# Kernel tuning notes

Hardware: AMD Instinct MI355X
Metric: run time of the kernel (lower is better)

## Reference

```python
import jax, jax.numpy as jnp
import numpy as np

H = 8
DK = 32
D_MODEL = H * DK


def _leaky(x):
    # LeakyReLU(negative_slope=0.1)
    return jnp.where(x > 0, x, 0.1 * x)


def _edge_feat(p_edge, W1, b1, W2, b2):
    # p_edge: [b, d_edge, n, n] -> [b, h, d_k, n, n]
    e = jnp.transpose(p_edge, (0, 2, 3, 1))          # [b, n, n, d_edge]
    e = _leaky(e @ W1 + b1) @ W2 + b2                # [b, n, n, d_model]
    b, n = e.shape[0], e.shape[1]
    e = e.reshape(b, n, n, H, DK)
    return jnp.transpose(e, (0, 3, 4, 1, 2))          # [b, h, d_k, n, n]


def setup_inputs() -> dict:
    key = jax.random.key(0)
    ks = jax.random.split(key, 24)
    b, n, d_model, d_edge, d_hidden = 2, 512, 256, 40, 32
    s = 0.05
    return {
        "query": jax.random.normal(ks[0], (b, n, d_model), jnp.float32),
        "key_": jax.random.normal(ks[1], (b, n, d_model), jnp.float32),
        "value": jax.random.normal(ks[2], (b, n, d_model), jnp.float32),
        "edges_att": jax.random.normal(ks[3], (b, d_edge, n, n), jnp.float32),
        "mask": jax.random.randint(ks[4], (b, n), 0, 2, jnp.int32),
        "Wq": jax.random.normal(ks[5], (d_model, d_model), jnp.float32) * s,
        "bq": jax.random.normal(ks[6], (d_model,), jnp.float32) * s,
        "Wk": jax.random.normal(ks[7], (d_model, d_model), jnp.float32) * s,
        "bk": jax.random.normal(ks[8], (d_model,), jnp.float32) * s,
        "Wv": jax.random.normal(ks[9], (d_model, d_model), jnp.float32) * s,
        "bv": jax.random.normal(ks[10], (d_model,), jnp.float32) * s,
        "Wo": jax.random.normal(ks[11], (d_model, d_model), jnp.float32) * s,
        "bo": jax.random.normal(ks[12], (d_model,), jnp.float32) * s,
        "rkW1": jax.random.normal(ks[13], (d_edge, d_hidden), jnp.float32) * s,
        "rkb1": jax.random.normal(ks[14], (d_hidden,), jnp.float32) * s,
        "rkW2": jax.random.normal(ks[15], (d_hidden, d_model), jnp.float32) * s,
        "rkb2": jax.random.normal(ks[16], (d_model,), jnp.float32) * s,
        "rvW1": jax.random.normal(ks[17], (d_edge, d_hidden), jnp.float32) * s,
        "rvb1": jax.random.normal(ks[18], (d_hidden,), jnp.float32) * s,
        "rvW2": jax.random.normal(ks[19], (d_hidden, d_model), jnp.float32) * s,
        "rvb2": jax.random.normal(ks[20], (d_model,), jnp.float32) * s,
        "u": jax.random.normal(ks[21], (H, DK), jnp.float32) * s,
        "v": jax.random.normal(ks[22], (H, DK), jnp.float32) * s,
    }


def reference(query, key_, value, edges_att, mask,
              Wq, bq, Wk, bk, Wv, bv, Wo, bo,
              rkW1, rkb1, rkW2, rkb2, rvW1, rvb1, rvW2, rvb2, u, v):
    b, n, _ = query.shape

    def proj(x, W, bb):
        return jnp.transpose((x @ W + bb).reshape(b, n, H, DK), (0, 2, 1, 3))  # [b,h,n,d_k]

    q = proj(query, Wq, bq)
    k = proj(key_, Wk, bk)
    val = proj(value, Wv, bv)

    relK = _edge_feat(edges_att, rkW1, rkb1, rkW2, rkb2)  # [b,h,d_k,n,n]
    relV = _edge_feat(edges_att, rvW1, rvb1, rvW2, rvb2)  # [b,h,d_k,n,n]

    inv = 1.0 / jnp.sqrt(jnp.asarray(DK, q.dtype))
    s1 = jnp.einsum('bhid,bhjd->bhij', q, k) * inv
    s2 = jnp.einsum('bhid,bhdij->bhij', q + k, relK) * inv
    s3 = jnp.einsum('bhid,hd->bhi', k, u)[..., None]      # broadcast over j
    s4 = jnp.einsum('bhdij,hd->bhij', relK, v)
    scores = s1 + s2 + s3 + s4
    scores = jnp.where(mask[:, None, None, :] == 0, jnp.asarray(-1e12, scores.dtype), scores)
    p = jax.nn.softmax(scores, axis=-1)                    # [b,h,n,n]

    o = jnp.einsum('bhij,bhjd->bhid', p, val) + jnp.einsum('bhij,bhdij->bhid', p, relV)
    x = jnp.transpose(o, (0, 2, 1, 3)).reshape(b, n, D_MODEL)
    return x @ Wo + bo
```

## Files before the change

kernel.cpp:

```cpp
#include <hip/hip_runtime.h>
#include <hip/hip_bf16.h>

#define HH 8
#define DKK 32
#define DM 256
#define NN 512
#define DE 40
#define DHID 32
#define CH 128

typedef __attribute__((ext_vector_type(4))) short short4v;
typedef __attribute__((ext_vector_type(8))) short short8v;
typedef __attribute__((ext_vector_type(4))) float f32x4;

__device__ __forceinline__ unsigned short f2bf(float x) {
    union { __hip_bfloat16 h; unsigned short u; } c;
    c.h = __float2bfloat16(x);
    return c.u;
}
__device__ __forceinline__ float bf2f(unsigned short u) {
    return __uint_as_float(((unsigned int)u) << 16);
}
__device__ __forceinline__ float bf_lo(unsigned int u){ return __uint_as_float(u << 16); }
__device__ __forceinline__ float bf_hi(unsigned int u){ return __uint_as_float(u & 0xffff0000u); }
__device__ __forceinline__ unsigned int pack2bf(float a, float b) {
    return (unsigned int)f2bf(a) | ((unsigned int)f2bf(b) << 16);
}
__device__ __forceinline__ short8v ld8(const unsigned short* p) {
    short4v lo = *(const short4v*)p;
    short4v hi = *(const short4v*)(p + 4);
    short8v r;
    r[0]=lo[0]; r[1]=lo[1]; r[2]=lo[2]; r[3]=lo[3];
    r[4]=hi[0]; r[5]=hi[1]; r[6]=hi[2]; r[7]=hi[3];
    return r;
}

__global__ __launch_bounds__(256) void w1_kernel(
    const float* __restrict__ rkW1, const float* __restrict__ rvW1,
    const float* __restrict__ rkb1, const float* __restrict__ rvb1,
    unsigned short* __restrict__ w1w, float* __restrict__ biasw)
{
    const int tid = threadIdx.x;
    const int n = tid >> 2, qd = tid & 3;
#pragma unroll
    for (int kk = 0; kk < 17; ++kk) {
        const int k = qd*17 + kk;
        float v = 0.f;
        if (k < DE) v = (n < 32) ? rkW1[k*DHID + n] : rvW1[k*DHID + (n-32)];
        w1w[n*68 + k] = f2bf(v);
    }
    if (tid < 64) biasw[tid] = (tid < 32) ? rkb1[tid] : rvb1[tid-32];
}

__global__ __launch_bounds__(256) void prep_kernel(
    const float* __restrict__ Q, const float* __restrict__ K,
    const float* __restrict__ vvec,
    const float* __restrict__ rkW2, const float* __restrict__ rkb2,
    float* __restrict__ gkw)
{
    const int bi = blockIdx.x;
    const int tid = threadIdx.x, h = tid >> 5, l32 = tid & 31;
    const float inv = 0.17677669529663687f;
    __shared__ __align__(16) float wf[DM];
    wf[tid] = inv*(Q[(size_t)bi*DM + tid] + K[(size_t)bi*DM + tid]) + vvec[tid];
    __syncthreads();
    float acc = 0.f;
#pragma unroll
    for (int d4 = 0; d4 < DKK/4; ++d4) {
        const float4 w4 = *(const float4*)(rkW2 + (size_t)l32*DM + h*DKK + d4*4);
        const float4 f4 = *(const float4*)(&wf[h*DKK + d4*4]);
        acc = fmaf(w4.x, f4.x, acc); acc = fmaf(w4.y, f4.y, acc);
        acc = fmaf(w4.z, f4.z, acc); acc = fmaf(w4.w, f4.w, acc);
    }
    gkw[(size_t)bi*264 + tid] = acc;
    if (tid < HH) {
        float a2 = 0.f;
#pragma unroll
        for (int d = 0; d < DKK; ++d)
            a2 = fmaf(rkb2[tid*DKK + d], wf[tid*DKK + d], a2);
        gkw[(size_t)bi*264 + 256 + tid] = a2;
    }
}

__global__ __launch_bounds__(256) void proj_kernel(
    const float* __restrict__ query, const float* __restrict__ key_,
    const float* __restrict__ value,
    const float* __restrict__ Wq, const float* __restrict__ bq,
    const float* __restrict__ Wk, const float* __restrict__ bk,
    const float* __restrict__ Wv, const float* __restrict__ bv,
    float* __restrict__ Q, float* __restrict__ K, float* __restrict__ V,
    int grpPerMat)
{
    const int m  = blockIdx.x / grpPerMat;
    const int r0 = (blockIdx.x % grpPerMat) * 4;
    const float* x; const float* W; const float* bb; float* dst;
    if (m == 0)      { x = query; W = Wq; bb = bq; dst = Q; }
    else if (m == 1) { x = key_;  W = Wk; bb = bk; dst = K; }
    else             { x = value; W = Wv; bb = bv; dst = V; }
    const int c = threadIdx.x;
    const float b0 = bb[c];
    float a0 = b0, a1 = b0, a2 = b0, a3 = b0;
    for (int k = 0; k < DM; ++k) {
        const float w = W[k*DM + c];
        a0 = fmaf(x[(size_t)(r0+0)*DM + k], w, a0);
        a1 = fmaf(x[(size_t)(r0+1)*DM + k], w, a1);
        a2 = fmaf(x[(size_t)(r0+2)*DM + k], w, a2);
        a3 = fmaf(x[(size_t)(r0+3)*DM + k], w, a3);
    }
    dst[(size_t)(r0+0)*DM + c] = a0;
    dst[(size_t)(r0+1)*DM + c] = a1;
    dst[(size_t)(r0+2)*DM + c] = a2;
    dst[(size_t)(r0+3)*DM + c] = a3;
}

__global__ __launch_bounds__(256) void s1_kernel(
    const float* __restrict__ Q, const float* __restrict__ K,
    unsigned short* __restrict__ s1)
{
    const int tid = threadIdx.x;
    const int bh = blockIdx.y, b = bh >> 3, hh = bh & 7;
    const int ti = (blockIdx.x >> 3) * 64, tj = (blockIdx.x & 7) * 64;
    __shared__ float Qt[64][33];
    __shared__ float Kt[64][33];
    const int c = tid & 31, r0 = tid >> 5;
#pragma unroll
    for (int s = 0; s < 8; ++s) {
        Qt[r0 + 8*s][c] = Q[(size_t)(b*NN + ti + r0 + 8*s)*DM + hh*DKK + c];
        Kt[r0 + 8*s][c] = K[(size_t)(b*NN + tj + r0 + 8*s)*DM + hh*DKK + c];
    }
    __syncthreads();
    const int tx = tid & 15, ty = tid >> 4;
    float acc[4][4] = {};
#pragma unroll
    for (int k = 0; k < DKK; ++k) {
        float qv[4], kv[4];
#pragma unroll
        for (int u = 0; u < 4; ++u) { qv[u] = Qt[ty*4+u][k]; kv[u] = Kt[tx*4+u][k]; }
#pragma unroll
        for (int ri = 0; ri < 4; ++ri)
#pragma unroll
            for (int cj = 0; cj < 4; ++cj)
                acc[ri][cj] = fmaf(qv[ri], kv[cj], acc[ri][cj]);
    }
    const float inv = 0.17677669529663687f;
#pragma unroll
    for (int ri = 0; ri < 4; ++ri) {
        ushort4 o;
        o.x = f2bf(acc[ri][0]*inv); o.y = f2bf(acc[ri][1]*inv);
        o.z = f2bf(acc[ri][2]*inv); o.w = f2bf(acc[ri][3]*inv);
        *(ushort4*)(s1 + ((size_t)(b*HH + hh)*NN + ti + ty*4 + ri)*NN + tj + tx*4) = o;
    }
}

__global__ __launch_bounds__(256, 5) void chunk_kernel(
    const float* __restrict__ edges, const int* __restrict__ mask,
    const float* __restrict__ vvec,
    const float* __restrict__ Q, const float* __restrict__ K, const float* __restrict__ V,
    const unsigned short* __restrict__ s1u,
    const unsigned short* __restrict__ w1w, const float* __restrict__ biasw,
    const float* __restrict__ gkw,
    float* __restrict__ ws_m, float* __restrict__ ws_z,
    float* __restrict__ ws_A, float* __restrict__ ws_O)
{
    const int bid = blockIdx.x;
    const int bi = bid >> 2, cq = bid & 3;
    const int b  = bi >> 9;
    const int i  = bi & 511;
    const int j0 = cq*CH;
    const int tid = threadIdx.x;
    const int h = tid >> 5, l32 = tid & 31;
    const int wid = tid >> 6, lane = tid & 63;
    const int g = lane >> 4, q16 = lane & 15;
    const int team = tid >> 6, qq = tid & 63, hq = qq >> 3;
    const int jj = tid & 127, half = tid >> 7;

    __shared__ __align__(16) unsigned char uni[17408];
    __shared__ __align__(16) unsigned short W1bf[64*68];
    __shared__ __align__(16) float sc[HH*132];
    __shared__ __align__(16) float gKs[HH*DKK];
    __shared__ float c0Ks[HH];
    __shared__ float bias_l[64];

    unsigned short* E   = (unsigned short*)uni;
    unsigned short* hvT = (unsigned short*)uni;
    unsigned short* hk  = (unsigned short*)(uni + 8448);
    unsigned short* pb  = (unsigned short*)(uni + 8448);
    float* paccA = (float*)uni;
    float* po    = (float*)(uni + 4096);

    const size_t ebase = (size_t)b*DE*NN*NN + (size_t)i*NN;

    float ev[20];
    {
        const float* ep = edges + ebase + j0 + jj;
#pragma unroll
        for (int u = 0; u < 20; ++u) ev[u] = ep[(size_t)(half*20+u)*NN*NN];
    }

    {
        const unsigned int* src = (const unsigned int*)w1w;
        unsigned int* dst = (unsigned int*)W1bf;
#pragma unroll
        for (int u = tid; u < 2176; u += 256) dst[u] = src[u];
        const float* gsrc = gkw + (size_t)bi*264;
        gKs[tid] = gsrc[tid];
        if (tid < HH) c0Ks[tid] = gsrc[256 + tid];
        if (tid < 64) bias_l[tid] = biasw[tid];
    }
    __syncthreads();

    float biasv[4];
#pragma unroll
    for (int nt = 0; nt < 4; ++nt) biasv[nt] = bias_l[nt*16 + q16];

    const float* vb = V + (size_t)b*NN*DM;
    const unsigned short* s1b = s1u + (size_t)b*HH*NN*NN + (size_t)i*NN;

    {
        unsigned int* Ed = (unsigned int*)&E[jj*68 + half*20];
#pragma unroll
        for (int u = 0; u < 10; ++u) Ed[u] = pack2bf(ev[2*u], ev[2*u+1]);
        if (half) {
            unsigned int* Ez = (unsigned int*)&E[jj*68 + 40];
#pragma unroll
            for (int z = 0; z < 12; ++z) Ez[z] = 0u;
        }
    }
    __syncthreads();

    f32x4 acc[2][4];
#pragma unroll
    for (int jt = 0; jt < 2; ++jt) {
        const int jn = wid*32 + jt*16 + q16;
        short8v a0 = ld8(&E[jn*68 + g*8]);
        short8v a1 = ld8(&E[jn*68 + 32 + g*8]);
#pragma unroll
        for (int nt = 0; nt < 4; ++nt) {
            const unsigned short* wp = &W1bf[(q16 + nt*16)*68 + g*8];
            f32x4 c;
            c[0] = biasv[nt]; c[1] = biasv[nt]; c[2] = biasv[nt]; c[3] = biasv[nt];
            c = __builtin_amdgcn_mfma_f32_16x16x32_bf16(a0, ld8(wp), c, 0, 0, 0);
            c = __builtin_amdgcn_mfma_f32_16x16x32_bf16(a1, ld8(wp + 32), c, 0, 0, 0);
            acc[jt][nt] = c;
        }
    }
    __syncthreads();

#pragma unroll
    for (int jt = 0; jt < 2; ++jt) {
        const int jw = wid*32 + jt*16 + g*4;
#pragma unroll
        for (int nt = 0; nt < 4; ++nt) {
#pragma unroll
            for (int r = 0; r < 4; ++r) {
                float x = acc[jt][nt][r];
                x = x > 0.f ? x : 0.1f*x;
                const unsigned short us = f2bf(x);
                const int n = nt*16 + q16;
                if (n < 32) hk[(jw+r)*34 + n] = us;
                else        hvT[(n-32)*132 + (jw+r)] = us;
            }
        }
    }
    __syncthreads();

    {
        unsigned int hku[16];
#pragma unroll
        for (int d = 0; d < 16; ++d) hku[d] = *(const unsigned int*)&hk[jj*34 + 2*d];
        const int mk = mask[b*NN + j0 + jj];
        float racc[4];
#pragma unroll
        for (int u = 0; u < 4; ++u) racc[u] = c0Ks[half*4 + u];
#pragma unroll
        for (int d = 0; d < 16; ++d) {
            const float lo = bf_lo(hku[d]), hi = bf_hi(hku[d]);
#pragma unroll
            for (int u = 0; u < 4; ++u) {
                const int hh = half*4 + u;
                racc[u] = fmaf(gKs[hh*DKK + 2*d],     lo, racc[u]);
                racc[u] = fmaf(gKs[hh*DKK + 2*d + 1], hi, racc[u]);
            }
        }
#pragma unroll
        for (int u = 0; u < 4; ++u) {
            const int hh = half*4 + u;
            float r = racc[u] + bf2f(s1b[(size_t)hh*NN*NN + j0 + jj]);
            if (mk == 0) r = -1e12f;
            sc[hh*132 + jj] = r;
        }
    }
    __syncthreads();

    {
        float sv[4];
        float mc = -3e38f;
#pragma unroll
        for (int k = 0; k < 4; ++k) { sv[k] = sc[h*132 + l32 + 32*k]; mc = fmaxf(mc, sv[k]); }
#pragma unroll
        for (int off = 16; off; off >>= 1) mc = fmaxf(mc, __shfl_xor(mc, off, 32));
        float zc = 0.f;
#pragma unroll
        for (int k = 0; k < 4; ++k) {
            const float e = __expf(sv[k] - mc);
            pb[h*132 + l32 + 32*k] = f2bf(e);
            zc += e;
        }
#pragma unroll
        for (int off = 16; off; off >>= 1) zc += __shfl_xor(zc, off, 32);
        if (l32 == 0) {
            ws_m[(size_t)bid*8 + h] = mc;
            ws_z[(size_t)bid*8 + h] = zc;
        }
    }
    __syncthreads();

    f32x4 accAf0 = {0.f,0.f,0.f,0.f}, accAf1 = {0.f,0.f,0.f,0.f};
    float aO0 = 0.f, aO1 = 0.f, aO2 = 0.f, aO3 = 0.f;
    {
        short8v pA = ld8(&pb[q16*132 + wid*32 + g*8]);
        short8v b0 = ld8(&hvT[q16*132 + wid*32 + g*8]);
        short8v b1 = ld8(&hvT[(16+q16)*132 + wid*32 + g*8]);
        accAf0 = __builtin_amdgcn_mfma_f32_16x16x32_bf16(pA, b0, accAf0, 0, 0, 0);
        accAf1 = __builtin_amdgcn_mfma_f32_16x16x32_bf16(pA, b1, accAf1, 0, 0, 0);

        const float* vrow = vb + (size_t)(j0 + team)*DM + qq*4;
        const unsigned short* ph = pb + hq*132 + team;
#pragma unroll 4
        for (int it = 0; it < 32; ++it) {
            const float p = bf2f(ph[4*it]);
            const float4 v4 = *(const float4*)(vrow + (size_t)it*4*DM);
            aO0 = fmaf(p, v4.x, aO0); aO1 = fmaf(p, v4.y, aO1);
            aO2 = fmaf(p, v4.z, aO2); aO3 = fmaf(p, v4.w, aO3);
        }
    }
    __syncthreads();

    if (g < 2) {
#pragma unroll
        for (int r = 0; r < 4; ++r) {
            paccA[wid*256 + (4*g+r)*32 + q16]      = accAf0[r];
            paccA[wid*256 + (4*g+r)*32 + 16 + q16] = accAf1[r];
        }
    }
    *(float4*)(po + team*256 + qq*4) = make_float4(aO0, aO1, aO2, aO3);
    __syncthreads();

    ws_A[(size_t)bid*256 + tid] = paccA[tid] + paccA[256+tid] + paccA[512+tid] + paccA[768+tid];
    ws_O[(size_t)bid*256 + tid] = po[tid] + po[256+tid] + po[512+tid] + po[768+tid];
}

__global__ __launch_bounds__(256) void combine_kernel(
    const float* __restrict__ rvW2, const float* __restrict__ rvb2,
    const float* __restrict__ Wo, const float* __restrict__ bo,
    const float* __restrict__ ws_m, const float* __restrict__ ws_z,
    const float* __restrict__ ws_A, const float* __restrict__ ws_O,
    float* __restrict__ out)
{
    const int bi0 = blockIdx.x * 2;
    const int tid = threadIdx.x;
    const int h = tid >> 5;
    __shared__ float A_l[2][DM], o_l[2][DM];
    __shared__ float wqs[2][4][HH], rzs[2][HH];

    if (tid < 16) {
        const int r = tid >> 3, hh = tid & 7;
        const int bi = bi0 + r;
        float mv[4], zv[4];
#pragma unroll
        for (int q = 0; q < 4; ++q) {
            mv[q] = ws_m[(size_t)(bi*4+q)*8 + hh];
            zv[q] = ws_z[(size_t)(bi*4+q)*8 + hh];
        }
        const float mm = fmaxf(fmaxf(mv[0], mv[1]), fmaxf(mv[2], mv[3]));
        float zt = 0.f;
#pragma unroll
        for (int q = 0; q < 4; ++q) {
            const float w = __expf(mv[q] - mm);
            wqs[r][q][hh] = w;
            zt = fmaf(zv[q], w, zt);
        }
        rzs[r][hh] = 1.f / zt;
    }
    __syncthreads();

    float o1v[2];
#pragma unroll
    for (int r = 0; r < 2; ++r) {
        const int bi = bi0 + r;
        const float rz = rzs[r][h];
        float A = 0.f, o1 = 0.f;
#pragma unroll
        for (int q = 0; q < 4; ++q) {
            const float w = wqs[r][q][h];
            A  = fmaf(w, ws_A[(size_t)(bi*4+q)*256 + tid], A);
            o1 = fmaf(w, ws_O[(size_t)(bi*4+q)*256 + tid], o1);
        }
        A_l[r][tid] = A * rz;
        o1v[r] = o1 * rz;
    }
    __syncthreads();

#pragma unroll
    for (int r = 0; r < 2; ++r) {
        float o2 = rvb2[tid];
#pragma unroll
        for (int t = 0; t < DHID; ++t)
            o2 = fmaf(A_l[r][h*DKK + t], rvW2[(size_t)t*DM + tid], o2);
        o_l[r][tid] = o1v[r] + o2;
    }
    __syncthreads();

    float acc0 = bo[tid], acc1 = acc0;
#pragma unroll 4
    for (int k = 0; k < DM; ++k) {
        const float w = Wo[(size_t)k*DM + tid];
        acc0 = fmaf(o_l[0][k], w, acc0);
        acc1 = fmaf(o_l[1][k], w, acc1);
    }
    out[(size_t)(bi0+0)*DM + tid] = acc0;
    out[(size_t)(bi0+1)*DM + tid] = acc1;
}

extern "C" void kernel_launch(void* const* d_in, const int* in_sizes, int n_in,
                              void* d_out, int out_size, void* d_ws, size_t ws_size,
                              hipStream_t stream) {
    const float* query = (const float*)d_in[0];
    const float* key_  = (const float*)d_in[1];
    const float* value = (const float*)d_in[2];
    const float* edges = (const float*)d_in[3];
    const int*   mask  = (const int*)d_in[4];
    const float* Wq = (const float*)d_in[5];
    const float* bq = (const float*)d_in[6];
    const float* Wk = (const float*)d_in[7];
    const float* bk = (const float*)d_in[8];
    const float* Wv = (const float*)d_in[9];
    const float* bv = (const float*)d_in[10];
    const float* Wo = (const float*)d_in[11];
    const float* bo = (const float*)d_in[12];
    const float* rkW1 = (const float*)d_in[13];
    const float* rkb1 = (const float*)d_in[14];
    const float* rkW2 = (const float*)d_in[15];
    const float* rkb2 = (const float*)d_in[16];
    const float* rvW1 = (const float*)d_in[17];
    const float* rvb1 = (const float*)d_in[18];
    const float* rvW2 = (const float*)d_in[19];
    const float* rvb2 = (const float*)d_in[20];
    const float* vvec = (const float*)d_in[22];

    const int rows = in_sizes[0] / DM;
    const int nchunk = rows * 4;

    float* Qw = (float*)d_ws;
    float* Kw = Qw + (size_t)rows*DM;
    float* Vw = Kw + (size_t)rows*DM;
    unsigned short* s1u = (unsigned short*)(Vw + (size_t)rows*DM);
    float* ws_m = (float*)(s1u + (size_t)2*HH*NN*NN);
    float* ws_z = ws_m + (size_t)nchunk*8;
    float* ws_A = ws_z + (size_t)nchunk*8;
    float* ws_O = ws_A + (size_t)nchunk*256;
    unsigned short* w1w = (unsigned short*)(ws_O + (size_t)nchunk*256);
    float* biasw = (float*)(w1w + 64*68 + 32);
    float* gkw   = biasw + 64;

    hipLaunchKernelGGL(w1_kernel, dim3(1), dim3(256), 0, stream,
                       rkW1, rvW1, rkb1, rvb1, w1w, biasw);
    hipLaunchKernelGGL(proj_kernel, dim3(3*rows/4), dim3(256), 0, stream,
                       query, key_, value, Wq, bq, Wk, bk, Wv, bv, Qw, Kw, Vw, rows/4);
    hipLaunchKernelGGL(s1_kernel, dim3(64, 16), dim3(256), 0, stream,
                       Qw, Kw, s1u);
    hipLaunchKernelGGL(prep_kernel, dim3(rows), dim3(256), 0, stream,
                       Qw, Kw, vvec, rkW2, rkb2, gkw);
    hipLaunchKernelGGL(chunk_kernel, dim3(nchunk), dim3(256), 0, stream,
                       edges, mask, vvec, Qw, Kw, Vw, s1u, w1w, biasw, gkw,
                       ws_m, ws_z, ws_A, ws_O);
    hipLaunchKernelGGL(combine_kernel, dim3(rows/2), dim3(256), 0, stream,
                       rvW2, rvb2, Wo, bo, ws_m, ws_z, ws_A, ws_O, (float*)d_out);
}
```

Measured before the change: 107.6 us.

## Split chunk kernel into edge-MLP stage and full-row attention with MFMA PV

Replaces the split-softmax chunk kernel plus combine kernel with two stages. The edge-MLP kernel writes full scores and the transposed hidden relV activations to workspace. A per-row attention kernel then does the exact softmax over all 512 keys and uses bf16 MFMA for P·V against a new transposed bf16 V written by the projection kernel. It also drops the W1 staging into LDS, reading weights directly from global. This trades the partial max/sum merge for extra global traffic of scores and hidden activations, and lowers V precision to bf16.

```diff
diff --git a/kernel.cpp b/kernel.cpp
--- a/kernel.cpp
+++ b/kernel.cpp
@@ -89,7 +89,7 @@
     const float* __restrict__ Wk, const float* __restrict__ bk,
     const float* __restrict__ Wv, const float* __restrict__ bv,
     float* __restrict__ Q, float* __restrict__ K, float* __restrict__ V,
-    int grpPerMat)
+    unsigned short* __restrict__ VbfT, int grpPerMat)
 {
     const int m  = blockIdx.x / grpPerMat;
     const int r0 = (blockIdx.x % grpPerMat) * 4;
@@ -111,6 +111,12 @@
     dst[(size_t)(r0+1)*DM + c] = a1;
     dst[(size_t)(r0+2)*DM + c] = a2;
     dst[(size_t)(r0+3)*DM + c] = a3;
+    if (m == 2) {
+        const int b = r0 >> 9, n0 = r0 & 511;
+        unsigned int* vt = (unsigned int*)(VbfT + ((size_t)(b*DM + c))*NN + n0);
+        vt[0] = pack2bf(a0, a1);
+        vt[1] = pack2bf(a2, a3);
+    }
 }
 
 __global__ __launch_bounds__(256) void s1_kernel(
@@ -152,41 +158,28 @@
     }
 }
 
-__global__ __launch_bounds__(256, 5) void chunk_kernel(
+__global__ __launch_bounds__(256, 5) void mlp_kernel(
     const float* __restrict__ edges, const int* __restrict__ mask,
-    const float* __restrict__ vvec,
-    const float* __restrict__ Q, const float* __restrict__ K, const float* __restrict__ V,
-    const unsigned short* __restrict__ s1u,
     const unsigned short* __restrict__ w1w, const float* __restrict__ biasw,
-    const float* __restrict__ gkw,
-    float* __restrict__ ws_m, float* __restrict__ ws_z,
-    float* __restrict__ ws_A, float* __restrict__ ws_O)
+    const float* __restrict__ gkw, const unsigned short* __restrict__ s1u,
+    float* __restrict__ s12, unsigned short* __restrict__ h1vT)
 {
     const int bid = blockIdx.x;
     const int bi = bid >> 2, cq = bid & 3;
-    const int b  = bi >> 9;
-    const int i  = bi & 511;
+    const int b  = bi >> 9, i = bi & 511;
     const int j0 = cq*CH;
     const int tid = threadIdx.x;
-    const int h = tid >> 5, l32 = tid & 31;
     const int wid = tid >> 6, lane = tid & 63;
     const int g = lane >> 4, q16 = lane & 15;
-    const int team = tid >> 6, qq = tid & 63, hq = qq >> 3;
     const int jj = tid & 127, half = tid >> 7;
 
     __shared__ __align__(16) unsigned char uni[17408];
-    __shared__ __align__(16) unsigned short W1bf[64*68];
-    __shared__ __align__(16) float sc[HH*132];
     __shared__ __align__(16) float gKs[HH*DKK];
     __shared__ float c0Ks[HH];
-    __shared__ float bias_l[64];
 
     unsigned short* E   = (unsigned short*)uni;
     unsigned short* hvT = (unsigned short*)uni;
     unsigned short* hk  = (unsigned short*)(uni + 8448);
-    unsigned short* pb  = (unsigned short*)(uni + 8448);
-    float* paccA = (float*)uni;
-    float* po    = (float*)(uni + 4096);
 
     const size_t ebase = (size_t)b*DE*NN*NN + (size_t)i*NN;
 
@@ -196,25 +189,14 @@
 #pragma unroll
         for (int u = 0; u < 20; ++u) ev[u] = ep[(size_t)(half*20+u)*NN*NN];
     }
-
-    {
-        const unsigned int* src = (const unsigned int*)w1w;
-        unsigned int* dst = (unsigned int*)W1bf;
-#pragma unroll
-        for (int u = tid; u < 2176; u += 256) dst[u] = src[u];
+    {
         const float* gsrc = gkw + (size_t)bi*264;
         gKs[tid] = gsrc[tid];
         if (tid < HH) c0Ks[tid] = gsrc[256 + tid];
-        if (tid < 64) bias_l[tid] = biasw[tid];
-    }
-    __syncthreads();
-
+    }
     float biasv[4];
 #pragma unroll
-    for (int nt = 0; nt < 4; ++nt) biasv[nt] = bias_l[nt*16 + q16];
-
-    const float* vb = V + (size_t)b*NN*DM;
-    const unsigned short* s1b = s1u + (size_t)b*HH*NN*NN + (size_t)i*NN;
+    for (int nt = 0; nt < 4; ++nt) biasv[nt] = biasw[nt*16 + q16];
 
     {
         unsigned int* Ed = (unsigned int*)&E[jj*68 + half*20];
@@ -236,7 +218,7 @@
         short8v a1 = ld8(&E[jn*68 + 32 + g*8]);
 #pragma unroll
         for (int nt = 0; nt < 4; ++nt) {
-            const unsigned short* wp = &W1bf[(q16 + nt*16)*68 + g*8];
+            const unsigned short* wp = w1w + (q16 + nt*16)*68 + g*8;
             f32x4 c;
             c[0] = biasv[nt]; c[1] = biasv[nt]; c[2] = biasv[nt]; c[3] = biasv[nt];
             c = __builtin_amdgcn_mfma_f32_16x16x32_bf16(a0, ld8(wp), c, 0, 0, 0);
@@ -269,6 +251,7 @@
 #pragma unroll
         for (int d = 0; d < 16; ++d) hku[d] = *(const unsigned int*)&hk[jj*34 + 2*d];
         const int mk = mask[b*NN + j0 + jj];
+        const unsigned short* s1b = s1u + (size_t)b*HH*NN*NN + (size_t)i*NN;
         float racc[4];
 #pragma unroll
         for (int u = 0; u < 4; ++u) racc[u] = c0Ks[half*4 + u];
@@ -287,139 +270,125 @@
             const int hh = half*4 + u;
             float r = racc[u] + bf2f(s1b[(size_t)hh*NN*NN + j0 + jj]);
             if (mk == 0) r = -1e12f;
-            sc[hh*132 + jj] = r;
-        }
-    }
-    __syncthreads();
-
-    {
-        float sv[4];
+            s12[(size_t)bi*4096 + hh*512 + j0 + jj] = r;
+        }
+    }
+    {
+        const int t = tid >> 3, c8 = tid & 7;
+        const unsigned int* src = (const unsigned int*)(hvT + t*132);
+        unsigned int* dst = (unsigned int*)(h1vT + ((size_t)bi*DHID + t)*NN + j0);
+#pragma unroll
+        for (int u = 0; u < 8; ++u) dst[c8*8 + u] = src[c8*8 + u];
+    }
+}
+
+__global__ __launch_bounds__(256, 4) void attn2_kernel(
+    const float* __restrict__ s12, const unsigned short* __restrict__ h1vT,
+    const unsigned short* __restrict__ VbfT,
+    const float* __restrict__ rvW2, const float* __restrict__ rvb2,
+    const float* __restrict__ Wo, const float* __restrict__ bo,
+    float* __restrict__ out)
+{
+    const int bi = blockIdx.x;
+    const int b  = bi >> 9;
+    const int tid = threadIdx.x;
+    const int h = tid >> 5, l32 = tid & 31;
+    const int wid = tid >> 6, lane = tid & 63;
+    const int g = lane >> 4, q16 = lane & 15;
+
+    __shared__ __align__(16) unsigned short pb[8*520];
+    __shared__ __align__(16) float paccA[4*256];
+    __shared__ __align__(16) float A_l[DM];
+    __shared__ __align__(16) float o_l[DM];
+    __shared__ float rz_s[HH];
+
+    {
+        float sv[16];
+        const float* srow = s12 + (size_t)bi*4096 + h*512 + l32;
+#pragma unroll
+        for (int k = 0; k < 16; ++k) sv[k] = srow[32*k];
         float mc = -3e38f;
 #pragma unroll
-        for (int k = 0; k < 4; ++k) { sv[k] = sc[h*132 + l32 + 32*k]; mc = fmaxf(mc, sv[k]); }
+        for (int k = 0; k < 16; ++k) mc = fmaxf(mc, sv[k]);
 #pragma unroll
         for (int off = 16; off; off >>= 1) mc = fmaxf(mc, __shfl_xor(mc, off, 32));
         float zc = 0.f;
 #pragma unroll
-        for (int k = 0; k < 4; ++k) {
+        for (int k = 0; k < 16; ++k) {
             const float e = __expf(sv[k] - mc);
-            pb[h*132 + l32 + 32*k] = f2bf(e);
+            pb[h*520 + l32 + 32*k] = f2bf(e);
             zc += e;
         }
 #pragma unroll
         for (int off = 16; off; off >>= 1) zc += __shfl_xor(zc, off, 32);
-        if (l32 == 0) {
-            ws_m[(size_t)bid*8 + h] = mc;
-            ws_z[(size_t)bid*8 + h] = zc;
-        }
-    }
-    __syncthreads();
-
-    f32x4 accAf0 = {0.f,0.f,0.f,0.f}, accAf1 = {0.f,0.f,0.f,0.f};
-    float aO0 = 0.f, aO1 = 0.f, aO2 = 0.f, aO3 = 0.f;
-    {
-        short8v pA = ld8(&pb[q16*132 + wid*32 + g*8]);
-        short8v b0 = ld8(&hvT[q16*132 + wid*32 + g*8]);
-        short8v b1 = ld8(&hvT[(16+q16)*132 + wid*32 + g*8]);
-        accAf0 = __builtin_amdgcn_mfma_f32_16x16x32_bf16(pA, b0, accAf0, 0, 0, 0);
-        accAf1 = __builtin_amdgcn_mfma_f32_16x16x32_bf16(pA, b1, accAf1, 0, 0, 0);
-
-        const float* vrow = vb + (size_t)(j0 + team)*DM + qq*4;
-        const unsigned short* ph = pb + hq*132 + team;
+        if (l32 == 0) rz_s[h] = 1.f / zc;
+    }
+    __syncthreads();
+
+    f32x4 co[4] = {{0,0,0,0},{0,0,0,0},{0,0,0,0},{0,0,0,0}};
+    f32x4 ca[2] = {{0,0,0,0},{0,0,0,0}};
+    {
+        const unsigned short* vbase = VbfT + (size_t)b*DM*NN;
 #pragma unroll 4
-        for (int it = 0; it < 32; ++it) {
-            const float p = bf2f(ph[4*it]);
-            const float4 v4 = *(const float4*)(vrow + (size_t)it*4*DM);
-            aO0 = fmaf(p, v4.x, aO0); aO1 = fmaf(p, v4.y, aO1);
-            aO2 = fmaf(p, v4.z, aO2); aO3 = fmaf(p, v4.w, aO3);
-        }
-    }
-    __syncthreads();
-
-    if (g < 2) {
-#pragma unroll
-        for (int r = 0; r < 4; ++r) {
-            paccA[wid*256 + (4*g+r)*32 + q16]      = accAf0[r];
-            paccA[wid*256 + (4*g+r)*32 + 16 + q16] = accAf1[r];
-        }
-    }
-    *(float4*)(po + team*256 + qq*4) = make_float4(aO0, aO1, aO2, aO3);
-    __syncthreads();
-
-    ws_A[(size_t)bid*256 + tid] = paccA[tid] + paccA[256+tid] + paccA[512+tid] + paccA[768+tid];
-    ws_O[(size_t)bid*256 + tid] = po[tid] + po[256+tid] + po[512+tid] + po[768+tid];
-}
-
-__global__ __launch_bounds__(256) void combine_kernel(
-    const float* __restrict__ rvW2, const float* __restrict__ rvb2,
-    const float* __restrict__ Wo, const float* __restrict__ bo,
-    const float* __restrict__ ws_m, const float* __restrict__ ws_z,
-    const float* __restrict__ ws_A, const float* __restrict__ ws_O,
-    float* __restrict__ out)
-{
-    const int bi0 = blockIdx.x * 2;
-    const int tid = threadIdx.x;
-    const int h = tid >> 5;
-    __shared__ float A_l[2][DM], o_l[2][DM];
-    __shared__ float wqs[2][4][HH], rzs[2][HH];
-
-    if (tid < 16) {
-        const int r = tid >> 3, hh = tid & 7;
-        const int bi = bi0 + r;
-        float mv[4], zv[4];
-#pragma unroll
-        for (int q = 0; q < 4; ++q) {
-            mv[q] = ws_m[(size_t)(bi*4+q)*8 + hh];
-            zv[q] = ws_z[(size_t)(bi*4+q)*8 + hh];
-        }
-        const float mm = fmaxf(fmaxf(mv[0], mv[1]), fmaxf(mv[2], mv[3]));
-        float zt = 0.f;
-#pragma unroll
-        for (int q = 0; q < 4; ++q) {
-            const float w = __expf(mv[q] - mm);
-            wqs[r][q][hh] = w;
-            zt = fmaf(zv[q], w, zt);
-        }
-        rzs[r][hh] = 1.f / zt;
-    }
-    __syncthreads();
-
-    float o1v[2];
-#pragma unroll
-    for (int r = 0; r < 2; ++r) {
-        const int bi = bi0 + r;
-        const float rz = rzs[r][h];
-        float A = 0.f, o1 = 0.f;
-#pragma unroll
-        for (int q = 0; q < 4; ++q) {
-            const float w = wqs[r][q][h];
-            A  = fmaf(w, ws_A[(size_t)(bi*4+q)*256 + tid], A);
-            o1 = fmaf(w, ws_O[(size_t)(bi*4+q)*256 + tid], o1);
-        }
-        A_l[r][tid] = A * rz;
-        o1v[r] = o1 * rz;
-    }
-    __syncthreads();
-
-#pragma unroll
-    for (int r = 0; r < 2; ++r) {
+        for (int ks = 0; ks < 16; ++ks) {
+            short8v pA = ld8(&pb[(lane & 7)*520 + ks*32 + g*8]);
+#pragma unroll
+            for (int nt = 0; nt < 4; ++nt) {
+                const int c = wid*64 + nt*16 + q16;
+                short8v bv = ld8(&vbase[(size_t)c*NN + ks*32 + g*8]);
+                co[nt] = __builtin_amdgcn_mfma_f32_16x16x32_bf16(pA, bv, co[nt], 0, 0, 0);
+            }
+        }
+        const unsigned short* habase = h1vT + (size_t)bi*DHID*NN;
+#pragma unroll
+        for (int kq = 0; kq < 4; ++kq) {
+            const int ks = wid*4 + kq;
+            short8v pA = ld8(&pb[(lane & 7)*520 + ks*32 + g*8]);
+#pragma unroll
+            for (int nt2 = 0; nt2 < 2; ++nt2) {
+                short8v hb = ld8(&habase[(size_t)(nt2*16 + q16)*NN + ks*32 + g*8]);
+                ca[nt2] = __builtin_amdgcn_mfma_f32_16x16x32_bf16(pA, hb, ca[nt2], 0, 0, 0);
+            }
+        }
+        if (g < 2) {
+#pragma unroll
+            for (int r = 0; r < 4; ++r) {
+                const int hrow = g*4 + r;
+                paccA[wid*256 + hrow*32 + q16]      = ca[0][r];
+                paccA[wid*256 + hrow*32 + 16 + q16] = ca[1][r];
+            }
+        }
+    }
+    __syncthreads();
+
+    A_l[tid] = (paccA[tid] + paccA[256+tid] + paccA[512+tid] + paccA[768+tid]) * rz_s[tid>>5];
+#pragma unroll
+    for (int nt = 0; nt < 4; ++nt) {
+        const int hc = wid*2 + (nt >> 1);
+        if (g == (hc >> 2)) {
+            const int c = wid*64 + nt*16 + q16;
+            o_l[c] = co[nt][hc & 3] * rz_s[hc];
+        }
+    }
+    __syncthreads();
+
+    {
         float o2 = rvb2[tid];
+        const int hb2 = tid >> 5;
 #pragma unroll
         for (int t = 0; t < DHID; ++t)
-            o2 = fmaf(A_l[r][h*DKK + t], rvW2[(size_t)t*DM + tid], o2);
-        o_l[r][tid] = o1v[r] + o2;
-    }
-    __syncthreads();
-
-    float acc0 = bo[tid], acc1 = acc0;
+            o2 = fmaf(A_l[hb2*DKK + t], rvW2[(size_t)t*DM + tid], o2);
+        o_l[tid] += o2;
+    }
+    __syncthreads();
+
+    {
+        float accw = bo[tid];
 #pragma unroll 4
-    for (int k = 0; k < DM; ++k) {
-        const float w = Wo[(size_t)k*DM + tid];
-        acc0 = fmaf(o_l[0][k], w, acc0);
-        acc1 = fmaf(o_l[1][k], w, acc1);
-    }
-    out[(size_t)(bi0+0)*DM + tid] = acc0;
-    out[(size_t)(bi0+1)*DM + tid] = acc1;
+        for (int k = 0; k < DM; ++k)
+            accw = fmaf(o_l[k], Wo[(size_t)k*DM + tid], accw);
+        out[(size_t)bi*DM + tid] = accw;
+    }
 }
 
 extern "C" void kernel_launch(void* const* d_in, const int* in_sizes, int n_in,
@@ -449,31 +418,29 @@
     const float* vvec = (const float*)d_in[22];
 
     const int rows = in_sizes[0] / DM;
-    const int nchunk = rows * 4;
-
-    float* Qw = (float*)d_ws;
-    float* Kw = Qw + (size_t)rows*DM;
-    float* Vw = Kw + (size_t)rows*DM;
-    unsigned short* s1u = (unsigned short*)(Vw + (size_t)rows*DM);
-    float* ws_m = (float*)(s1u + (size_t)2*HH*NN*NN);
-    float* ws_z = ws_m + (size_t)nchunk*8;
-    float* ws_A = ws_z + (size_t)nchunk*8;
-    float* ws_O = ws_A + (size_t)nchunk*256;
-    unsigned short* w1w = (unsigned short*)(ws_O + (size_t)nchunk*256);
-    float* biasw = (float*)(w1w + 64*68 + 32);
+
+    float* Qw   = (float*)d_ws;
+    float* Kw   = Qw  + (size_t)rows*DM;
+    float* Vw   = Kw  + (size_t)rows*DM;
+    float* s12w = Vw  + (size_t)rows*DM;
+    float* biasw = s12w + (size_t)rows*4096;
     float* gkw   = biasw + 64;
+    unsigned short* s1u  = (unsigned short*)(gkw + (size_t)rows*264);
+    unsigned short* VbfT = s1u + (size_t)2*HH*NN*NN;
+    unsigned short* w1w  = VbfT + (size_t)2*DM*NN;
+    unsigned short* h1vT = w1w + 64*68;
 
     hipLaunchKernelGGL(w1_kernel, dim3(1), dim3(256), 0, stream,
                        rkW1, rvW1, rkb1, rvb1, w1w, biasw);
     hipLaunchKernelGGL(proj_kernel, dim3(3*rows/4), dim3(256), 0, stream,
-                       query, key_, value, Wq, bq, Wk, bk, Wv, bv, Qw, Kw, Vw, rows/4);
+                       query, key_, value, Wq, bq, Wk, bk, Wv, bv,
+                       Qw, Kw, Vw, VbfT, rows/4);
     hipLaunchKernelGGL(s1_kernel, dim3(64, 16), dim3(256), 0, stream,
                        Qw, Kw, s1u);
     hipLaunchKernelGGL(prep_kernel, dim3(rows), dim3(256), 0, stream,
                        Qw, Kw, vvec, rkW2, rkb2, gkw);
-    hipLaunchKernelGGL(chunk_kernel, dim3(nchunk), dim3(256), 0, stream,
-                       edges, mask, vvec, Qw, Kw, Vw, s1u, w1w, biasw, gkw,
-                       ws_m, ws_z, ws_A, ws_O);
-    hipLaunchKernelGGL(combine_kernel, dim3(rows/2), dim3(256), 0, stream,
-                       rvW2, rvb2, Wo, bo, ws_m, ws_z, ws_A, ws_O, (float*)d_out);
-}
+    hipLaunchKernelGGL(mlp_kernel, dim3(rows*4), dim3(256), 0, stream,
+                       edges, mask, w1w, biasw, gkw, s1u, s12w, h1vT);
+    hipLaunchKernelGGL(attn2_kernel, dim3(rows), dim3(256), 0, stream,
+                       s12w, h1vT, VbfT, rvW2, rvb2, Wo, bo, (float*)d_out);
+}
```

Result: slower. 125.5 us (+16.6%).

## Use MFMA for P·V with transposed bf16 V and merge prep kernels

Applied to the files above, without the earlier changes.

The projection kernel now also writes V as a transposed bf16 array. The chunk kernel computes the per-head P·V product with bf16 MFMA over that array, replacing the scalar fp32 FMA loop and its shared-memory reduction; only the diagonal head blocks are stored. The s1, prep and w1 kernels are merged into one launch that picks its role by block index, saving two launches. The MFMA path computes all heads against all value columns and discards off-diagonal blocks, and bf16 V lowers precision.

```diff
diff --git a/kernel.cpp b/kernel.cpp
--- a/kernel.cpp
+++ b/kernel.cpp
@@ -35,53 +35,6 @@
     return r;
 }
 
-__global__ __launch_bounds__(256) void w1_kernel(
-    const float* __restrict__ rkW1, const float* __restrict__ rvW1,
-    const float* __restrict__ rkb1, const float* __restrict__ rvb1,
-    unsigned short* __restrict__ w1w, float* __restrict__ biasw)
-{
-    const int tid = threadIdx.x;
-    const int n = tid >> 2, qd = tid & 3;
-#pragma unroll
-    for (int kk = 0; kk < 17; ++kk) {
-        const int k = qd*17 + kk;
-        float v = 0.f;
-        if (k < DE) v = (n < 32) ? rkW1[k*DHID + n] : rvW1[k*DHID + (n-32)];
-        w1w[n*68 + k] = f2bf(v);
-    }
-    if (tid < 64) biasw[tid] = (tid < 32) ? rkb1[tid] : rvb1[tid-32];
-}
-
-__global__ __launch_bounds__(256) void prep_kernel(
-    const float* __restrict__ Q, const float* __restrict__ K,
-    const float* __restrict__ vvec,
-    const float* __restrict__ rkW2, const float* __restrict__ rkb2,
-    float* __restrict__ gkw)
-{
-    const int bi = blockIdx.x;
-    const int tid = threadIdx.x, h = tid >> 5, l32 = tid & 31;
-    const float inv = 0.17677669529663687f;
-    __shared__ __align__(16) float wf[DM];
-    wf[tid] = inv*(Q[(size_t)bi*DM + tid] + K[(size_t)bi*DM + tid]) + vvec[tid];
-    __syncthreads();
-    float acc = 0.f;
-#pragma unroll
-    for (int d4 = 0; d4 < DKK/4; ++d4) {
-        const float4 w4 = *(const float4*)(rkW2 + (size_t)l32*DM + h*DKK + d4*4);
-        const float4 f4 = *(const float4*)(&wf[h*DKK + d4*4]);
-        acc = fmaf(w4.x, f4.x, acc); acc = fmaf(w4.y, f4.y, acc);
-        acc = fmaf(w4.z, f4.z, acc); acc = fmaf(w4.w, f4.w, acc);
-    }
-    gkw[(size_t)bi*264 + tid] = acc;
-    if (tid < HH) {
-        float a2 = 0.f;
-#pragma unroll
-        for (int d = 0; d < DKK; ++d)
-            a2 = fmaf(rkb2[tid*DKK + d], wf[tid*DKK + d], a2);
-        gkw[(size_t)bi*264 + 256 + tid] = a2;
-    }
-}
-
 __global__ __launch_bounds__(256) void proj_kernel(
     const float* __restrict__ query, const float* __restrict__ key_,
     const float* __restrict__ value,
@@ -89,7 +42,7 @@
     const float* __restrict__ Wk, const float* __restrict__ bk,
     const float* __restrict__ Wv, const float* __restrict__ bv,
     float* __restrict__ Q, float* __restrict__ K, float* __restrict__ V,
-    int grpPerMat)
+    unsigned short* __restrict__ VbfT, int grpPerMat)
 {
     const int m  = blockIdx.x / grpPerMat;
     const int r0 = (blockIdx.x % grpPerMat) * 4;
@@ -111,51 +64,100 @@
     dst[(size_t)(r0+1)*DM + c] = a1;
     dst[(size_t)(r0+2)*DM + c] = a2;
     dst[(size_t)(r0+3)*DM + c] = a3;
-}
-
-__global__ __launch_bounds__(256) void s1_kernel(
+    if (m == 2) {
+        const int b = r0 >> 9, n0 = r0 & 511;
+        unsigned int* vt = (unsigned int*)(VbfT + ((size_t)(b*DM + c))*NN + n0);
+        vt[0] = pack2bf(a0, a1);
+        vt[1] = pack2bf(a2, a3);
+    }
+}
+
+__global__ __launch_bounds__(256) void pre_kernel(
     const float* __restrict__ Q, const float* __restrict__ K,
-    unsigned short* __restrict__ s1)
+    const float* __restrict__ vvec,
+    const float* __restrict__ rkW2, const float* __restrict__ rkb2,
+    const float* __restrict__ rkW1, const float* __restrict__ rvW1,
+    const float* __restrict__ rkb1, const float* __restrict__ rvb1,
+    unsigned short* __restrict__ s1, float* __restrict__ gkw,
+    unsigned short* __restrict__ w1w, float* __restrict__ biasw)
 {
+    const int bid = blockIdx.x;
     const int tid = threadIdx.x;
-    const int bh = blockIdx.y, b = bh >> 3, hh = bh & 7;
-    const int ti = (blockIdx.x >> 3) * 64, tj = (blockIdx.x & 7) * 64;
-    __shared__ float Qt[64][33];
-    __shared__ float Kt[64][33];
-    const int c = tid & 31, r0 = tid >> 5;
-#pragma unroll
-    for (int s = 0; s < 8; ++s) {
-        Qt[r0 + 8*s][c] = Q[(size_t)(b*NN + ti + r0 + 8*s)*DM + hh*DKK + c];
-        Kt[r0 + 8*s][c] = K[(size_t)(b*NN + tj + r0 + 8*s)*DM + hh*DKK + c];
-    }
-    __syncthreads();
-    const int tx = tid & 15, ty = tid >> 4;
-    float acc[4][4] = {};
-#pragma unroll
-    for (int k = 0; k < DKK; ++k) {
-        float qv[4], kv[4];
-#pragma unroll
-        for (int u = 0; u < 4; ++u) { qv[u] = Qt[ty*4+u][k]; kv[u] = Kt[tx*4+u][k]; }
-#pragma unroll
-        for (int ri = 0; ri < 4; ++ri)
-#pragma unroll
-            for (int cj = 0; cj < 4; ++cj)
-                acc[ri][cj] = fmaf(qv[ri], kv[cj], acc[ri][cj]);
-    }
-    const float inv = 0.17677669529663687f;
-#pragma unroll
-    for (int ri = 0; ri < 4; ++ri) {
-        ushort4 o;
-        o.x = f2bf(acc[ri][0]*inv); o.y = f2bf(acc[ri][1]*inv);
-        o.z = f2bf(acc[ri][2]*inv); o.w = f2bf(acc[ri][3]*inv);
-        *(ushort4*)(s1 + ((size_t)(b*HH + hh)*NN + ti + ty*4 + ri)*NN + tj + tx*4) = o;
+    __shared__ __align__(16) float sh[2*64*33];
+
+    if (bid < 1024) {
+        float (*Qt)[33] = (float(*)[33])sh;
+        float (*Kt)[33] = (float(*)[33])(sh + 64*33);
+        const int bh = bid >> 6, b = bh >> 3, hh = bh & 7;
+        const int bx = bid & 63;
+        const int ti = (bx >> 3) * 64, tj = (bx & 7) * 64;
+        const int c = tid & 31, r0 = tid >> 5;
+#pragma unroll
+        for (int s = 0; s < 8; ++s) {
+            Qt[r0 + 8*s][c] = Q[(size_t)(b*NN + ti + r0 + 8*s)*DM + hh*DKK + c];
+            Kt[r0 + 8*s][c] = K[(size_t)(b*NN + tj + r0 + 8*s)*DM + hh*DKK + c];
+        }
+        __syncthreads();
+        const int tx = tid & 15, ty = tid >> 4;
+        float acc[4][4] = {};
+#pragma unroll
+        for (int k = 0; k < DKK; ++k) {
+            float qv[4], kv[4];
+#pragma unroll
+            for (int u = 0; u < 4; ++u) { qv[u] = Qt[ty*4+u][k]; kv[u] = Kt[tx*4+u][k]; }
+#pragma unroll
+            for (int ri = 0; ri < 4; ++ri)
+#pragma unroll
+                for (int cj = 0; cj < 4; ++cj)
+                    acc[ri][cj] = fmaf(qv[ri], kv[cj], acc[ri][cj]);
+        }
+        const float inv = 0.17677669529663687f;
+#pragma unroll
+        for (int ri = 0; ri < 4; ++ri) {
+            ushort4 o;
+            o.x = f2bf(acc[ri][0]*inv); o.y = f2bf(acc[ri][1]*inv);
+            o.z = f2bf(acc[ri][2]*inv); o.w = f2bf(acc[ri][3]*inv);
+            *(ushort4*)(s1 + ((size_t)(b*HH + hh)*NN + ti + ty*4 + ri)*NN + tj + tx*4) = o;
+        }
+    } else if (bid < 2048) {
+        const int bi = bid - 1024;
+        const int h = tid >> 5, l32 = tid & 31;
+        const float inv = 0.17677669529663687f;
+        float* wf = sh;
+        wf[tid] = inv*(Q[(size_t)bi*DM + tid] + K[(size_t)bi*DM + tid]) + vvec[tid];
+        __syncthreads();
+        float acc = 0.f;
+#pragma unroll
+        for (int d4 = 0; d4 < DKK/4; ++d4) {
+            const float4 w4 = *(const float4*)(rkW2 + (size_t)l32*DM + h*DKK + d4*4);
+            const float4 f4 = *(const float4*)(&wf[h*DKK + d4*4]);
+            acc = fmaf(w4.x, f4.x, acc); acc = fmaf(w4.y, f4.y, acc);
+            acc = fmaf(w4.z, f4.z, acc); acc = fmaf(w4.w, f4.w, acc);
+        }
+        gkw[(size_t)bi*264 + tid] = acc;
+        if (tid < HH) {
+            float a2 = 0.f;
+#pragma unroll
+            for (int d = 0; d < DKK; ++d)
+                a2 = fmaf(rkb2[tid*DKK + d], wf[tid*DKK + d], a2);
+            gkw[(size_t)bi*264 + 256 + tid] = a2;
+        }
+    } else {
+        const int n = tid >> 2, qd = tid & 3;
+#pragma unroll
+        for (int kk = 0; kk < 17; ++kk) {
+            const int k = qd*17 + kk;
+            float v = 0.f;
+            if (k < DE) v = (n < 32) ? rkW1[k*DHID + n] : rvW1[k*DHID + (n-32)];
+            w1w[n*68 + k] = f2bf(v);
+        }
+        if (tid < 64) biasw[tid] = (tid < 32) ? rkb1[tid] : rvb1[tid-32];
     }
 }
 
 __global__ __launch_bounds__(256, 5) void chunk_kernel(
     const float* __restrict__ edges, const int* __restrict__ mask,
-    const float* __restrict__ vvec,
-    const float* __restrict__ Q, const float* __restrict__ K, const float* __restrict__ V,
+    const unsigned short* __restrict__ VbfT,
     const unsigned short* __restrict__ s1u,
     const unsigned short* __restrict__ w1w, const float* __restrict__ biasw,
     const float* __restrict__ gkw,
@@ -171,7 +173,6 @@
     const int h = tid >> 5, l32 = tid & 31;
     const int wid = tid >> 6, lane = tid & 63;
     const int g = lane >> 4, q16 = lane & 15;
-    const int team = tid >> 6, qq = tid & 63, hq = qq >> 3;
     const int jj = tid & 127, half = tid >> 7;
 
     __shared__ __align__(16) unsigned char uni[17408];
@@ -186,7 +187,6 @@
     unsigned short* hk  = (unsigned short*)(uni + 8448);
     unsigned short* pb  = (unsigned short*)(uni + 8448);
     float* paccA = (float*)uni;
-    float* po    = (float*)(uni + 4096);
 
     const size_t ebase = (size_t)b*DE*NN*NN + (size_t)i*NN;
 
@@ -213,7 +213,7 @@
 #pragma unroll
     for (int nt = 0; nt < 4; ++nt) biasv[nt] = bias_l[nt*16 + q16];
 
-    const float* vb = V + (size_t)b*NN*DM;
+    const unsigned short* vtb = VbfT + (size_t)b*DM*NN;
     const unsigned short* s1b = s1u + (size_t)b*HH*NN*NN + (size_t)i*NN;
 
     {
@@ -315,23 +315,35 @@
     }
     __syncthreads();
 
-    f32x4 accAf0 = {0.f,0.f,0.f,0.f}, accAf1 = {0.f,0.f,0.f,0.f};
-    float aO0 = 0.f, aO1 = 0.f, aO2 = 0.f, aO3 = 0.f;
+    f32x4 ca0 = {0.f,0.f,0.f,0.f}, ca1 = {0.f,0.f,0.f,0.f};
     {
         short8v pA = ld8(&pb[q16*132 + wid*32 + g*8]);
         short8v b0 = ld8(&hvT[q16*132 + wid*32 + g*8]);
         short8v b1 = ld8(&hvT[(16+q16)*132 + wid*32 + g*8]);
-        accAf0 = __builtin_amdgcn_mfma_f32_16x16x32_bf16(pA, b0, accAf0, 0, 0, 0);
-        accAf1 = __builtin_amdgcn_mfma_f32_16x16x32_bf16(pA, b1, accAf1, 0, 0, 0);
-
-        const float* vrow = vb + (size_t)(j0 + team)*DM + qq*4;
-        const unsigned short* ph = pb + hq*132 + team;
-#pragma unroll 4
-        for (int it = 0; it < 32; ++it) {
-            const float p = bf2f(ph[4*it]);
-            const float4 v4 = *(const float4*)(vrow + (size_t)it*4*DM);
-            aO0 = fmaf(p, v4.x, aO0); aO1 = fmaf(p, v4.y, aO1);
-            aO2 = fmaf(p, v4.z, aO2); aO3 = fmaf(p, v4.w, aO3);
+        ca0 = __builtin_amdgcn_mfma_f32_16x16x32_bf16(pA, b0, ca0, 0, 0, 0);
+        ca1 = __builtin_amdgcn_mfma_f32_16x16x32_bf16(pA, b1, ca1, 0, 0, 0);
+    }
+
+    {
+        f32x4 co[4] = {{0,0,0,0},{0,0,0,0},{0,0,0,0},{0,0,0,0}};
+#pragma unroll
+        for (int ks = 0; ks < 4; ++ks) {
+            short8v pB = ld8(&pb[q16*132 + ks*32 + g*8]);
+#pragma unroll
+            for (int t = 0; t < 4; ++t) {
+                const int c_row = (wid<<6) + (t<<4) + q16;
+                short8v aV = ld8(&vtb[(size_t)c_row*NN + j0 + ks*32 + g*8]);
+                co[t] = __builtin_amdgcn_mfma_f32_16x16x32_bf16(aV, pB, co[t], 0, 0, 0);
+            }
+        }
+#pragma unroll
+        for (int t = 0; t < 4; ++t) {
+            const int hstar = wid*2 + (t >> 1);
+            if (q16 == hstar) {
+#pragma unroll
+                for (int r = 0; r < 4; ++r)
+                    ws_O[(size_t)bid*256 + (wid<<6) + (t<<4) + (g<<2) + r] = co[t][r];
+            }
         }
     }
     __syncthreads();
@@ -339,15 +351,13 @@
     if (g < 2) {
 #pragma unroll
         for (int r = 0; r < 4; ++r) {
-            paccA[wid*256 + (4*g+r)*32 + q16]      = accAf0[r];
-            paccA[wid*256 + (4*g+r)*32 + 16 + q16] = accAf1[r];
-        }
-    }
-    *(float4*)(po + team*256 + qq*4) = make_float4(aO0, aO1, aO2, aO3);
-    __syncthreads();
-
+            const int hrow = g*4 + r;
+            paccA[wid*256 + hrow*32 + q16]      = ca0[r];
+            paccA[wid*256 + hrow*32 + 16 + q16] = ca1[r];
+        }
+    }
+    __syncthreads();
     ws_A[(size_t)bid*256 + tid] = paccA[tid] + paccA[256+tid] + paccA[512+tid] + paccA[768+tid];
-    ws_O[(size_t)bid*256 + tid] = po[tid] + po[256+tid] + po[512+tid] + po[768+tid];
 }
 
 __global__ __launch_bounds__(256) void combine_kernel(
@@ -451,28 +461,27 @@
     const int rows = in_sizes[0] / DM;
     const int nchunk = rows * 4;
 
-    float* Qw = (float*)d_ws;
-    float* Kw = Qw + (size_t)rows*DM;
-    float* Vw = Kw + (size_t)rows*DM;
-    unsigned short* s1u = (unsigned short*)(Vw + (size_t)rows*DM);
-    float* ws_m = (float*)(s1u + (size_t)2*HH*NN*NN);
+    float* Qw   = (float*)d_ws;
+    float* Kw   = Qw + (size_t)rows*DM;
+    float* Vw   = Kw + (size_t)rows*DM;
+    float* gkw  = Vw + (size_t)rows*DM;
+    float* biasw = gkw + (size_t)rows*264;
+    float* ws_m = biasw + 64;
     float* ws_z = ws_m + (size_t)nchunk*8;
     float* ws_A = ws_z + (size_t)nchunk*8;
     float* ws_O = ws_A + (size_t)nchunk*256;
-    unsigned short* w1w = (unsigned short*)(ws_O + (size_t)nchunk*256);
-    float* biasw = (float*)(w1w + 64*68 + 32);
-    float* gkw   = biasw + 64;
-
-    hipLaunchKernelGGL(w1_kernel, dim3(1), dim3(256), 0, stream,
-                       rkW1, rvW1, rkb1, rvb1, w1w, biasw);
+    unsigned short* s1u  = (unsigned short*)(ws_O + (size_t)nchunk*256);
+    unsigned short* VbfT = s1u + (size_t)2*HH*NN*NN;
+    unsigned short* w1w  = VbfT + (size_t)2*DM*NN;
+
     hipLaunchKernelGGL(proj_kernel, dim3(3*rows/4), dim3(256), 0, stream,
-                       query, key_, value, Wq, bq, Wk, bk, Wv, bv, Qw, Kw, Vw, rows/4);
-    hipLaunchKernelGGL(s1_kernel, dim3(64, 16), dim3(256), 0, stream,
-                       Qw, Kw, s1u);
-    hipLaunchKernelGGL(prep_kernel, dim3(rows), dim3(256), 0, stream,
-                       Qw, Kw, vvec, rkW2, rkb2, gkw);
+                       query, key_, value, Wq, bq, Wk, bk, Wv, bv,
+                       Qw, Kw, Vw, VbfT, rows/4);
+    hipLaunchKernelGGL(pre_kernel, dim3(2*rows + 1), dim3(256), 0, stream,
+                       Qw, Kw, vvec, rkW2, rkb2, rkW1, rvW1, rkb1, rvb1,
+                       s1u, gkw, w1w, biasw);
     hipLaunchKernelGGL(chunk_kernel, dim3(nchunk), dim3(256), 0, stream,
-                       edges, mask, vvec, Qw, Kw, Vw, s1u, w1w, biasw, gkw,
+                       edges, mask, VbfT, s1u, w1w, biasw, gkw,
                        ws_m, ws_z, ws_A, ws_O);
     hipLaunchKernelGGL(combine_kernel, dim3(rows/2), dim3(256), 0, stream,
                        rvW2, rvb2, Wo, bo, ws_m, ws_z, ws_A, ws_O, (float*)d_out);
```

Measured after the change: 115.6 us. 1.07x slower.
